# Performance work log

Hardware: AMD Instinct MI355X
Metric: run time of the kernel (lower is better)

Reference implementation:

```python
import jax, jax.numpy as jnp
import numpy as np

N_NODES = 10000
N_EDGES = 160000


def _conv2d(x, w, b):
    y = jax.lax.conv_general_dilated(x, w, (1, 1), 'SAME',
                                     dimension_numbers=('NCHW', 'OIHW', 'NCHW'))
    return jax.nn.selu(y + b[None, :, None, None])


def _cnn(cf, cnn_w1, cnn_b1, cnn_w2, cnn_b2, cnn_w3, cnn_b3, cnn_w4, cnn_b4):
    h = _conv2d(cf, cnn_w1, cnn_b1)
    h = _conv2d(h, cnn_w2, cnn_b2)
    h = _conv2d(h, cnn_w3, cnn_b3)
    h = _conv2d(h, cnn_w4, cnn_b4)
    return h.mean(axis=(2, 3))  # (1, 24) global avg pool


def _gat(x, src, dst, W, a_s, a_d, b, n):
    # PyG GATConv, concat=False (mean over heads), add_self_loops handled by caller
    H, C = a_s.shape
    h = (x @ W).reshape(-1, H, C)                      # (N,H,C)
    e = jax.nn.leaky_relu((h * a_s).sum(-1)[src] +
                          (h * a_d).sum(-1)[dst], 0.2)  # (E,H)
    m = jax.ops.segment_max(e, dst, num_segments=n)
    p = jnp.exp(e - m[dst])
    z = jax.ops.segment_sum(p, dst, num_segments=n)
    alpha = p / (z[dst] + 1e-16)
    out = jax.ops.segment_sum(h[src] * alpha[..., None], dst, num_segments=n)
    return out.mean(axis=1) + b


def _fix_boundary(v, up, down, left, right):
    c0 = jnp.where(down, 0.0, jnp.where(up, 1.0, v[:, 0]))
    c1 = jnp.where(right, 1.0, jnp.where(left, 0.0, v[:, 1]))
    return v.at[:, 0].set(c0).at[:, 1].set(c1)


def setup_inputs() -> dict:
    key = jax.random.key(0)
    ks = jax.random.split(key, 40)
    d = {}
    d['x'] = jax.random.uniform(ks[0], (N_NODES, 10), dtype=jnp.float32)
    d['edge_index'] = jax.random.randint(ks[1], (2, N_EDGES), 0, N_NODES, dtype=jnp.int64)
    d['conv_feat'] = jax.random.normal(ks[2], (1, 4, 64, 64), dtype=jnp.float32)
    cnn_dims = [(16, 4), (32, 16), (64, 32), (24, 64)]
    for i, (o, c) in enumerate(cnn_dims, 1):
        d[f'cnn_w{i}'] = jax.random.normal(ks[2 + i], (o, c, 3, 3), jnp.float32) * 0.1
        d[f'cnn_b{i}'] = jnp.zeros((o,), jnp.float32)
    gat_dims = [(34, 8, 64), (64, 16, 128), (128, 8, 256), (256, 8, 128), (128, 16, 2)]
    for i, (fin, H, C) in enumerate(gat_dims, 1):
        k1, k2, k3 = jax.random.split(ks[10 + i], 3)
        d[f'g{i}_w'] = jax.random.normal(k1, (fin, H * C), jnp.float32) * 0.1
        d[f'g{i}_as'] = jax.random.normal(k2, (H, C), jnp.float32) * 0.1
        d[f'g{i}_ad'] = jax.random.normal(k3, (H, C), jnp.float32) * 0.1
        d[f'g{i}_b'] = jnp.zeros((C,), jnp.float32)
    return d


def reference(x, edge_index, conv_feat,
              cnn_w1, cnn_b1, cnn_w2, cnn_b2, cnn_w3, cnn_b3, cnn_w4, cnn_b4,
              g1_w, g1_as, g1_ad, g1_b,
              g2_w, g2_as, g2_ad, g2_b,
              g3_w, g3_as, g3_ad, g3_b,
              g4_w, g4_as, g4_ad, g4_b,
              g5_w, g5_as, g5_ad, g5_b):
    n = x.shape[0]
    # boundary masks from raw node coordinates
    up, down = x[:, 0] == 1, x[:, 0] == 0
    left, right = x[:, 1] == 0, x[:, 1] == 1
    # add self loops (PyG GATConv default)
    loops = jnp.arange(n, dtype=edge_index.dtype)
    src = jnp.concatenate([edge_index[0], loops])
    dst = jnp.concatenate([edge_index[1], loops])

    gfeat = _cnn(conv_feat, cnn_w1, cnn_b1, cnn_w2, cnn_b2, cnn_w3, cnn_b3, cnn_w4, cnn_b4)
    h = jnp.concatenate([jnp.broadcast_to(gfeat, (n, gfeat.shape[1])), x], axis=1)

    h = jax.nn.selu(_gat(h, src, dst, g1_w, g1_as, g1_ad, g1_b, n))
    h = _fix_boundary(h, up, down, left, right)
    h = jax.nn.selu(_gat(h, src, dst, g2_w, g2_as, g2_ad, g2_b, n))
    h = _fix_boundary(h, up, down, left, right)
    h = jax.nn.selu(_gat(h, src, dst, g3_w, g3_as, g3_ad, g3_b, n))
    h = _fix_boundary(h, up, down, left, right)
    h = jax.nn.selu(_gat(h, src, dst, g4_w, g4_as, g4_ad, g4_b, n))
    h = _fix_boundary(h, up, down, left, right)
    res = jax.nn.selu(_gat(h, src, dst, g5_w, g5_as, g5_ad, g5_b, n))
    out = x[:, :2] + res
    out = _fix_boundary(out, up, down, left, right)
    return out
```

## Files before the change

### kernel.cpp

```cpp
#include <hip/hip_runtime.h>
#include <hip/hip_fp16.h>
#include <math.h>


#define DEVFN static __device__ __forceinline__

typedef __attribute__((ext_vector_type(8))) _Float16 half8;
typedef __attribute__((ext_vector_type(4))) _Float16 half4v;
typedef __attribute__((ext_vector_type(4))) float f32x4;

DEVFN float selu_f(float v) {
    const float scale = 1.0507009873554805f;
    const float alpha = 1.6732632423543772f;
    return v > 0.f ? scale * v : scale * alpha * (expf(v) - 1.f);
}

DEVFN float lrelu02(float v) { return v > 0.f ? v : 0.2f * v; }

#define PST 66
#define PSZ (66 * 66)

__global__ void pad_input(const float* __restrict__ cf, float* __restrict__ out) {
    int t = blockIdx.x * blockDim.x + threadIdx.x;
    if (t >= 4 * 4096) return;
    int c = t >> 12, pix = t & 4095;
    int y = pix >> 6, x = pix & 63;
    out[c * PSZ + (y + 1) * PST + (x + 1)] = cf[t];
}

template <int CIN>
__global__ __launch_bounds__(256) void conv3x3_pad(const float* __restrict__ in,
                                                   const float* __restrict__ w,
                                                   const float* __restrict__ b,
                                                   float* __restrict__ out) {
    int x  = threadIdx.x & 63;
    int yg = threadIdx.x >> 6;
    int y  = blockIdx.x * 4 + yg;
    int co = blockIdx.y;
    float acc = b[co];
    const float* wp = w + (size_t)co * CIN * 9;
#pragma unroll 4
    for (int ci = 0; ci < CIN; ++ci) {
        const float* ip = in + ci * PSZ + y * PST + x;
        const float* wr = wp + ci * 9;
        acc += wr[0] * ip[0]           + wr[1] * ip[1]           + wr[2] * ip[2]
             + wr[3] * ip[PST]         + wr[4] * ip[PST + 1]     + wr[5] * ip[PST + 2]
             + wr[6] * ip[2 * PST]     + wr[7] * ip[2 * PST + 1] + wr[8] * ip[2 * PST + 2];
    }
    out[(size_t)co * PSZ + (y + 1) * PST + (x + 1)] = selu_f(acc);
}

__global__ void avgpool_c(const float* __restrict__ in, float* __restrict__ gfeat) {
    int c = blockIdx.x;
    int t = threadIdx.x;
    float s = 0.f;
    for (int i = t; i < 4096; i += 256) {
        int y = i >> 6, x = i & 63;
        s += in[c * PSZ + (y + 1) * PST + (x + 1)];
    }
#pragma unroll
    for (int off = 32; off >= 1; off >>= 1) s += __shfl_xor(s, off);
    __shared__ float red[4];
    int wave = t >> 6, lane = t & 63;
    if (lane == 0) red[wave] = s;
    __syncthreads();
    if (t == 0) gfeat[c] = (red[0] + red[1] + red[2] + red[3]) * (1.f / 4096.f);
}

__global__ void build_h0(const float* __restrict__ x, const float* __restrict__ gfeat,
                         __half* __restrict__ h0f, unsigned* __restrict__ masks, int N) {
    int n = blockIdx.x * blockDim.x + threadIdx.x;
    if (n >= N) return;
    float x0 = x[n * 10 + 0], x1 = x[n * 10 + 1];
    unsigned mk = (x0 == 1.f ? 1u : 0u) | (x0 == 0.f ? 2u : 0u) |
                  (x1 == 0.f ? 4u : 0u) | (x1 == 1.f ? 8u : 0u);
    masks[n] = mk;
    __half* hq = h0f + (size_t)n * 64;
#pragma unroll
    for (int j = 0; j < 64; ++j) {
        float v = (j < 24) ? gfeat[j] : (j < 34 ? x[n * 10 + (j - 24)] : 0.f);
        hq[j] = __float2half(v);
    }
}

__global__ void count_dst(const int* __restrict__ ei, int* __restrict__ cnt, int E, int N) {
    int t = blockIdx.x * blockDim.x + threadIdx.x;
    if (t >= E + N) return;
    int dst = (t < E) ? ei[E + t] : (t - E);
    atomicAdd(&cnt[dst], 1);
}

__global__ void scan_blocks(const int* __restrict__ cnt, int* __restrict__ pref,
                            int* __restrict__ bsums, int n) {
    __shared__ int sdata[256];
    int i = blockIdx.x * 256 + threadIdx.x;
    int v = (i < n) ? cnt[i] : 0;
    sdata[threadIdx.x] = v;
    __syncthreads();
    for (int off = 1; off < 256; off <<= 1) {
        int tmp = (threadIdx.x >= off) ? sdata[threadIdx.x - off] : 0;
        __syncthreads();
        sdata[threadIdx.x] += tmp;
        __syncthreads();
    }
    if (i < n) pref[i] = sdata[threadIdx.x] - v;
    if (threadIdx.x == 255) bsums[blockIdx.x] = sdata[255];
}

__global__ void scan_sums(int* __restrict__ bsums, int nb) {
    int tid = threadIdx.x;
    int orig = (tid < nb) ? bsums[tid] : 0;
    int v = orig;
#pragma unroll
    for (int off = 1; off < 64; off <<= 1) {
        int u = __shfl_up(v, off);
        if (tid >= off) v += u;
    }
    if (tid < nb) bsums[tid] = v - orig;
}

__global__ void scan_apply(const int* __restrict__ pref, const int* __restrict__ bsums,
                           int* __restrict__ indptr, int* __restrict__ cursor,
                           int n, int total) {
    int i = blockIdx.x * 256 + threadIdx.x;
    if (i == 0) indptr[n] = total;
    if (i >= n) return;
    int e = bsums[blockIdx.x] + pref[i];
    indptr[i] = e;
    cursor[i] = e;
}

__global__ void scatter_edges(const int* __restrict__ ei, int* __restrict__ cursor,
                              int* __restrict__ col, int E, int N) {
    int t = blockIdx.x * blockDim.x + threadIdx.x;
    if (t >= E + N) return;
    int src, dst;
    if (t < E) { src = ei[t]; dst = ei[E + t]; }
    else       { src = dst = t - E; }
    int pos = atomicAdd(&cursor[dst], 1);
    col[pos] = src;
}

__global__ __launch_bounds__(256) void prep_all(
        const float* __restrict__ W0, const float* __restrict__ W1,
        const float* __restrict__ W2, const float* __restrict__ W3,
        const float* __restrict__ W4,
        const float* __restrict__ as0, const float* __restrict__ as1,
        const float* __restrict__ as2, const float* __restrict__ as3,
        const float* __restrict__ as4,
        const float* __restrict__ ad0, const float* __restrict__ ad1,
        const float* __restrict__ ad2, const float* __restrict__ ad3,
        const float* __restrict__ ad4,
        unsigned short* __restrict__ bt, float* __restrict__ wesed,
        float* __restrict__ wcomb) {
    const int Kc[5]  = {34, 64, 128, 256, 128};
    const int Kpc[5] = {64, 64, 128, 256, 128};
    const int Hc[5]  = {8, 16, 8, 8, 16};
    const int Cc[5]  = {64, 128, 256, 128, 2};
    const int HCc[5] = {512, 2048, 2048, 1024, 32};
    const int KAc[5] = {512, 1024, 1024, 2048, 2048};
    const int btOff[5] = {0, 32768, 163840, 425984, 0};
    const int weOff[5] = {0, 1024, 3072, 5120, 9216};

    int b = blockIdx.x, tid = threadIdx.x;

    if (b < 168) {
        int lyr, tloc;
        if (b < 8)        { lyr = 0; tloc = b; }
        else if (b < 40)  { lyr = 1; tloc = b - 8; }
        else if (b < 104) { lyr = 2; tloc = b - 40; }
        else              { lyr = 3; tloc = b - 104; }
        const int ktl[4] = {1, 1, 2, 4};
        const int mtl[4] = {1, 2, 4, 2};
        int kt = ktl[lyr], mt = mtl[lyr];
        int per_h = kt * mt;
        int h = tloc / per_h, r = tloc - h * per_h;
        int ki = r % kt, mi = r / kt;
        int k0 = ki * 64, m0 = mi * 64;
        int K = Kc[lyr], Kp = Kpc[lyr], C = Cc[lyr], HC = HCc[lyr], KA = KAc[lyr];
        const float* W;
        if (lyr == 0) W = W0; else if (lyr == 1) W = W1;
        else if (lyr == 2) W = W2; else W = W3;

        __shared__ float tile[64][65];
        int c = tid & 63, rg = tid >> 6;
        for (int r2 = rg; r2 < 64; r2 += 4) {
            int k = k0 + r2, m = m0 + c;
            float v = (k < K && m < C) ? W[(size_t)k * HC + h * C + m] : 0.f;
            tile[r2][c] = v;
        }
        __syncthreads();
        unsigned short* bp = bt + btOff[lyr];
        for (int mr = rg; mr < 64; mr += 4) {
            int m = m0 + mr, k = k0 + c;
            if (m < C && k < Kp)
                bp[(size_t)m * KA + h * Kp + k] =
                    __half_as_ushort(__float2half(tile[c][mr]));
        }
    } else if (b < 200) {
        int u = (b - 168) * 256 + tid;
        int k = u >> 6, o = u & 63;
        float s;
        if (o < 32) {
            int h = (o < 16) ? o : o - 16;
            const float* av = ((o < 16) ? as4 : ad4) + h * 2;
            s = W4[k * 32 + h * 2 + 0] * av[0] + W4[k * 32 + h * 2 + 1] * av[1];
        } else {
            s = W4[k * 32 + (o - 32)];
        }
        wcomb[u] = s;
    } else {
        int wb = b - 200;
        int lyr, u0;
        if (wb < 4)       { lyr = 0; u0 = wb * 256; }
        else if (wb < 12) { lyr = 1; u0 = (wb - 4) * 256; }
        else if (wb < 20) { lyr = 2; u0 = (wb - 12) * 256; }
        else if (wb < 36) { lyr = 3; u0 = (wb - 20) * 256; }
        else              { lyr = 4; u0 = (wb - 36) * 256; }
        int u = u0 + tid;
        int K = Kc[lyr], Kp = Kpc[lyr], H = Hc[lyr], C = Cc[lyr], HC = HCc[lyr];
        int H2 = 2 * H;
        if (u < Kp * H2) {
            int k = u / H2, o = u - k * H2;
            float s = 0.f;
            if (k < K) {
                int h = (o < H) ? o : o - H;
                const float *W, *as_, *ad_;
                if (lyr == 0)      { W = W0; as_ = as0; ad_ = ad0; }
                else if (lyr == 1) { W = W1; as_ = as1; ad_ = ad1; }
                else if (lyr == 2) { W = W2; as_ = as2; ad_ = ad2; }
                else if (lyr == 3) { W = W3; as_ = as3; ad_ = ad3; }
                else               { W = W4; as_ = as4; ad_ = ad4; }
                const float* av = ((o < H) ? as_ : ad_) + h * C;
                const float* wp = W + (size_t)k * HC + h * C;
#pragma unroll 4
                for (int c2 = 0; c2 < C; ++c2) s += wp[c2] * av[c2];
            }
            wesed[weOff[lyr] + u] = s;
        }
    }
}

__global__ void esed_kernel(const __half* __restrict__ hin, const float* __restrict__ wesed,
                            float* __restrict__ esed, int N, int Kp, int H2) {
    int t = blockIdx.x * blockDim.x + threadIdx.x;
    if (t >= N * H2) return;
    int n = t / H2, o = t - n * H2;
    const __half2* hp = (const __half2*)(hin + (size_t)n * Kp);
    float s = 0.f;
    for (int k2 = 0; k2 < Kp / 2; ++k2) {
        float2 f = __half22float2(hp[k2]);
        s += f.x * wesed[(2 * k2) * H2 + o] + f.y * wesed[(2 * k2 + 1) * H2 + o];
    }
    esed[t] = s;
}

template <int H, int KP, int CH, int NPB>
__global__ __launch_bounds__(NPB * (KP / CH)) void gat_fused_lds(
        const __half* __restrict__ hinf, const float* __restrict__ esed,
        const int* __restrict__ indptr, const int* __restrict__ col,
        __half* __restrict__ g, int N) {
    const int TPN = KP / CH;
    const int EC  = TPN / H;
    const int H2  = 2 * H;
    __shared__ float lds_p[NPB][TPN];
    int sub = threadIdx.x / TPN;
    int j   = threadIdx.x % TPN;
    int n = blockIdx.x * NPB + sub;
    if (n >= N) return;
    int e_my = j / H, h_my = j % H;
    int c0 = j * CH;
    float edv = esed[n * H2 + H + h_my];

    float acc[H][CH];
#pragma unroll
    for (int h = 0; h < H; ++h)
#pragma unroll
        for (int t = 0; t < CH; ++t) acc[h][t] = 0.f;
    float zloc = 0.f;

    int beg = indptr[n], deg = indptr[n + 1] - beg;
    for (int base = 0; base < deg; base += EC) {
        int ce = base + e_my;
        float p = 0.f;
        if (ce < deg) {
            int srcm = col[beg + ce];
            p = expf(lrelu02(esed[srcm * H2 + h_my] + edv));
        }
        zloc += p;
        lds_p[sub][j] = p;
        __builtin_amdgcn_wave_barrier();
#pragma unroll
        for (int e = 0; e < EC; ++e) {
            int idx = base + e;
            if (idx < deg) {
                int src = col[beg + idx];
                float f[CH];
                if (CH == 2) {
                    __half2 hv = *(const __half2*)(hinf + (size_t)src * KP + c0);
                    float2 ff = __half22float2(hv);
                    f[0] = ff.x; f[1] = ff.y;
                } else {
                    half4v hv = *(const half4v*)(hinf + (size_t)src * KP + c0);
                    f[0] = (float)hv[0]; f[1] = (float)hv[1];
                    f[2] = (float)hv[2]; f[3] = (float)hv[3];
                }
                const float4* ap = (const float4*)&lds_p[sub][e * H];
#pragma unroll
                for (int q4 = 0; q4 < H / 4; ++q4) {
                    float4 a4 = ap[q4];
#pragma unroll
                    for (int t = 0; t < CH; ++t) {
                        acc[4 * q4 + 0][t] += a4.x * f[t];
                        acc[4 * q4 + 1][t] += a4.y * f[t];
                        acc[4 * q4 + 2][t] += a4.z * f[t];
                        acc[4 * q4 + 3][t] += a4.w * f[t];
                    }
                }
            }
        }
        __builtin_amdgcn_wave_barrier();
    }

#pragma unroll
    for (int off = H; off < TPN; off <<= 1)
        zloc += __shfl_xor(zloc, off, TPN);
    float zinv_my = (1.f / H) / (zloc + 1e-16f);

    __half* gp = g + (size_t)n * (H * KP) + c0;
#pragma unroll
    for (int h = 0; h < H; ++h) {
        float zf = __shfl(zinv_my, h, TPN);
        if (CH == 2) {
            *(__half2*)(gp + h * KP) =
                __floats2half2_rn(acc[h][0] * zf, acc[h][1] * zf);
        } else {
            __half2 lo = __floats2half2_rn(acc[h][0] * zf, acc[h][1] * zf);
            __half2 hi = __floats2half2_rn(acc[h][2] * zf, acc[h][3] * zf);
            union { __half2 h2[2]; float2 f2; } u;
            u.h2[0] = lo; u.h2[1] = hi;
            *(float2*)(gp + h * KP) = u.f2;
        }
    }
}

template <int NPB>
__global__ __launch_bounds__(NPB * 32) void final_attn(
        const float* __restrict__ eyp, const int* __restrict__ indptr,
        const int* __restrict__ col, const float* __restrict__ b5,
        const unsigned* __restrict__ masks, const float* __restrict__ x,
        float* __restrict__ outp, int N) {
    int sub = threadIdx.x >> 5;
    int j   = threadIdx.x & 31;
    int n = blockIdx.x * NPB + sub;
    if (n >= N) return;
    int h = j >> 1;
    float edv = eyp[(size_t)n * 64 + 16 + h];
    int beg = indptr[n], end = indptr[n + 1];
    float z = 0.f, a = 0.f;
    int i = beg;
    for (; i + 1 < end; i += 2) {
        int s0 = col[i], s1 = col[i + 1];
        const float* r0 = eyp + (size_t)s0 * 64;
        const float* r1 = eyp + (size_t)s1 * 64;
        float es0 = r0[h], y0 = r0[32 + j];
        float es1 = r1[h], y1 = r1[32 + j];
        float p0 = expf(lrelu02(es0 + edv));
        float p1 = expf(lrelu02(es1 + edv));
        z += p0; a += p0 * y0;
        z += p1; a += p1 * y1;
    }
    for (; i < end; ++i) {
        const float* r = eyp + (size_t)col[i] * 64;
        float p = expf(lrelu02(r[h] + edv));
        z += p; a += p * r[32 + j];
    }
    float zf = (1.f / 16.f) / (z + 1e-16f);
    float val = a * zf;
#pragma unroll
    for (int off = 2; off <= 16; off <<= 1) val += __shfl_xor(val, off, 32);
    float other = __shfl_xor(val, 1, 32);
    if (j == 0) {
        unsigned mk = masks[n];
        float v0 = x[n * 10 + 0] + selu_f(val + b5[0]);
        float v1 = x[n * 10 + 1] + selu_f(other + b5[1]);
        if (mk & 2u) v0 = 0.f; else if (mk & 1u) v0 = 1.f;
        if (mk & 8u) v1 = 1.f; else if (mk & 4u) v1 = 0.f;
        outp[n * 2 + 0] = v0;
        outp[n * 2 + 1] = v1;
    }
}

#define LDP 72
__global__ __launch_bounds__(256) void gemm_lds(const __half* __restrict__ A,
                                                const unsigned short* __restrict__ Bhi,
                                                const float* __restrict__ bias,
                                                const unsigned* __restrict__ masks,
                                                __half* __restrict__ O16,
                                                int N, int K, int M) {
    __shared__ __half lA[64 * LDP], lB[64 * LDP];
    int tid = threadIdx.x;
    int wave = tid >> 6, lane = tid & 63;
    int ln16 = lane & 15, q = lane >> 4;
    int row0 = blockIdx.x * 64;
    int col0 = blockIdx.y * 64;

    int r0 = tid >> 3, r1 = r0 + 32;
    int ac = (tid & 7) * 8;
    int ga0 = min(row0 + r0, N - 1);
    int ga1 = min(row0 + r1, N - 1);
    const __half* Bp = (const __half*)Bhi;
    const __half* a0p = A + (size_t)ga0 * K + ac;
    const __half* a1p = A + (size_t)ga1 * K + ac;
    const __half* b0p = Bp + (size_t)(col0 + r0) * K + ac;
    const __half* b1p = Bp + (size_t)(col0 + r1) * K + ac;

    half8 ra0 = *(const half8*)(a0p);
    half8 ra1 = *(const half8*)(a1p);
    half8 rb0 = *(const half8*)(b0p);
    half8 rb1 = *(const half8*)(b1p);

    f32x4 acc[4];
#pragma unroll
    for (int j = 0; j < 4; ++j) acc[j] = (f32x4){0.f, 0.f, 0.f, 0.f};

    for (int kc = 0; kc < K; kc += 64) {
        __syncthreads();
        *(half8*)(lA + r0 * LDP + ac) = ra0;
        *(half8*)(lA + r1 * LDP + ac) = ra1;
        *(half8*)(lB + r0 * LDP + ac) = rb0;
        *(half8*)(lB + r1 * LDP + ac) = rb1;
        __syncthreads();
        int kn = kc + 64;
        if (kn < K) {
            ra0 = *(const half8*)(a0p + kn);
            ra1 = *(const half8*)(a1p + kn);
            rb0 = *(const half8*)(b0p + kn);
            rb1 = *(const half8*)(b1p + kn);
        }
#pragma unroll
        for (int kk = 0; kk < 2; ++kk) {
            half8 af = *(const half8*)(lA + (wave * 16 + ln16) * LDP + kk * 32 + q * 8);
#pragma unroll
            for (int j = 0; j < 4; ++j) {
                half8 bf = *(const half8*)(lB + (j * 16 + ln16) * LDP + kk * 32 + q * 8);
                acc[j] = __builtin_amdgcn_mfma_f32_16x16x32_f16(af, bf, acc[j], 0, 0, 0);
            }
        }
    }

#pragma unroll
    for (int j = 0; j < 4; ++j) {
        int cc = col0 + j * 16 + ln16;
        float bv = bias[cc];
#pragma unroll
        for (int r = 0; r < 4; ++r) {
            int rr = row0 + wave * 16 + q * 4 + r;
            if (rr >= N) continue;
            float v = selu_f(acc[j][r] + bv);
            if (cc < 2) {
                unsigned mk = masks[rr];
                if (cc == 0) { if (mk & 2u) v = 0.f; else if (mk & 1u) v = 1.f; }
                else         { if (mk & 8u) v = 1.f; else if (mk & 4u) v = 0.f; }
            }
            O16[(size_t)rr * M + cc] = __float2half(v);
        }
    }
}

extern "C" void kernel_launch(void* const* d_in, const int* in_sizes, int n_in,
                              void* d_out, int out_size, void* d_ws, size_t ws_size,
                              hipStream_t stream) {
    const float* x   = (const float*)d_in[0];
    const int*   ei  = (const int*)d_in[1];
    const float* cf  = (const float*)d_in[2];
    const float* cw[4] = {(const float*)d_in[3], (const float*)d_in[5],
                          (const float*)d_in[7], (const float*)d_in[9]};
    const float* cb[4] = {(const float*)d_in[4], (const float*)d_in[6],
                          (const float*)d_in[8], (const float*)d_in[10]};
    const float* gw[5], *gas[5], *gad[5], *gb[5];
    for (int i = 0; i < 5; ++i) {
        gw[i]  = (const float*)d_in[11 + 4 * i];
        gas[i] = (const float*)d_in[12 + 4 * i];
        gad[i] = (const float*)d_in[13 + 4 * i];
        gb[i]  = (const float*)d_in[14 + 4 * i];
    }
    const int N = in_sizes[0] / 10;
    const int E = in_sizes[1] / 2;
    const int EN = E + N;
    const int NB = (N + 255) / 256;

    char* base = (char*)d_ws;
    size_t off = 0;
    auto alloc = [&](size_t bytes) -> char* {
        char* p = base + off;
        off = (off + bytes + 255) & ~(size_t)255;
        return p;
    };
    float* cfp   = (float*)alloc((size_t)4 * PSZ * 4);
    float* c1p   = (float*)alloc((size_t)16 * PSZ * 4);
    float* c2p   = (float*)alloc((size_t)32 * PSZ * 4);
    float* c3p   = (float*)alloc((size_t)64 * PSZ * 4);
    float* c4p   = (float*)alloc((size_t)24 * PSZ * 4);
    float* gfeat = (float*)alloc(24 * 4);
    __half* hA16 = (__half*)alloc((size_t)N * 256 * 2);
    __half* hB16 = (__half*)alloc((size_t)N * 256 * 2);
    __half* g    = (__half*)alloc((size_t)N * 2048 * 2);
    float* esed  = (float*)alloc((size_t)N * 32 * 4);
    float* eyp   = (float*)alloc((size_t)N * 64 * 4);
    float* wesed = (float*)alloc((size_t)13312 * 4);
    float* wcomb = (float*)alloc((size_t)8192 * 4);
    unsigned short* bt = (unsigned short*)alloc((size_t)688128 * 2);
    unsigned* masks = (unsigned*)alloc((size_t)N * 4);
    int* cnt    = (int*)alloc((size_t)N * 4);
    int* pref   = (int*)alloc((size_t)N * 4);
    int* bsums  = (int*)alloc(64 * 4);
    int* indptr = (int*)alloc((size_t)(N + 1) * 4);
    int* cursor = (int*)alloc((size_t)N * 4);
    int* col    = (int*)alloc((size_t)EN * 4);
    (void)ws_size;

    prep_all<<<252, 256, 0, stream>>>(gw[0], gw[1], gw[2], gw[3], gw[4],
                                      gas[0], gas[1], gas[2], gas[3], gas[4],
                                      gad[0], gad[1], gad[2], gad[3], gad[4],
                                      bt, wesed, wcomb);

    hipMemsetAsync(cfp, 0, (size_t)140 * PSZ * 4, stream);
    pad_input<<<(4 * 4096 + 255) / 256, 256, 0, stream>>>(cf, cfp);
    conv3x3_pad<4><<<dim3(16, 16), 256, 0, stream>>>(cfp, cw[0], cb[0], c1p);
    conv3x3_pad<16><<<dim3(16, 32), 256, 0, stream>>>(c1p, cw[1], cb[1], c2p);
    conv3x3_pad<32><<<dim3(16, 64), 256, 0, stream>>>(c2p, cw[2], cb[2], c3p);
    conv3x3_pad<64><<<dim3(16, 24), 256, 0, stream>>>(c3p, cw[3], cb[3], c4p);
    avgpool_c<<<24, 256, 0, stream>>>(c4p, gfeat);

    build_h0<<<(N + 255) / 256, 256, 0, stream>>>(x, gfeat, hA16, masks, N);

    hipMemsetAsync(cnt, 0, (size_t)N * 4, stream);
    count_dst<<<(EN + 255) / 256, 256, 0, stream>>>(ei, cnt, E, N);
    scan_blocks<<<NB, 256, 0, stream>>>(cnt, pref, bsums, N);
    scan_sums<<<1, 64, 0, stream>>>(bsums, NB);
    scan_apply<<<NB, 256, 0, stream>>>(pref, bsums, indptr, cursor, N, EN);
    scatter_edges<<<(EN + 255) / 256, 256, 0, stream>>>(ei, cursor, col, E, N);

    const int Hs[5] = {8, 16, 8, 8, 16};
    const int Cs[5] = {64, 128, 256, 128, 2};
    const int Kp[5] = {64, 64, 128, 256, 128};
    const int btOffA[5] = {0, 32768, 163840, 425984, 0};
    const int weOffA[5] = {0, 1024, 3072, 5120, 9216};

    const __half* hin16 = hA16;
    __half* hout16[4]  = {hB16, hA16, hB16, hA16};

    for (int lyr = 0; lyr < 5; ++lyr) {
        int KP = Kp[lyr], H = Hs[lyr], C = Cs[lyr];
        int KA = H * KP;
        if (lyr == 4) {
            esed_kernel<<<(N * 64 + 255) / 256, 256, 0, stream>>>(hin16, wcomb, eyp,
                                                                  N, 128, 64);
            final_attn<8><<<(N + 7) / 8, 256, 0, stream>>>(eyp, indptr, col, gb[4],
                                                           masks, x, (float*)d_out, N);
            break;
        }
        esed_kernel<<<(N * 2 * H + 255) / 256, 256, 0, stream>>>(hin16, wesed + weOffA[lyr],
                                                                 esed, N, KP, 2 * H);
        if (lyr == 0) {
            gat_fused_lds<8, 64, 4, 16><<<(N + 15) / 16, 256, 0, stream>>>(
                hin16, esed, indptr, col, g, N);
        } else if (lyr == 1) {
            gat_fused_lds<16, 64, 2, 8><<<(N + 7) / 8, 256, 0, stream>>>(
                hin16, esed, indptr, col, g, N);
        } else if (lyr == 2) {
            gat_fused_lds<8, 128, 4, 8><<<(N + 7) / 8, 256, 0, stream>>>(
                hin16, esed, indptr, col, g, N);
        } else {
            gat_fused_lds<8, 256, 4, 4><<<(N + 3) / 4, 256, 0, stream>>>(
                hin16, esed, indptr, col, g, N);
        }

        const unsigned short* btL = bt + btOffA[lyr];
        int gx = (N + 63) / 64;
        gemm_lds<<<dim3(gx, C / 64), 256, 0, stream>>>(g, btL, gb[lyr], masks,
                                                       hout16[lyr], N, KA, C);
        hin16 = hout16[lyr];
    }
}
```

Baseline: 513.1 us.

## Double-buffer attention weights in GAT aggregation and add 32x128 GEMM tile

The GAT aggregation kernel now double-buffers the per-edge attention coefficients in LDS. It prefetches the next chunk's source index and score before the current chunk's feature accumulation, so load latency overlaps with FMA work and one wave barrier per iteration goes away. A new GEMM kernel with 32-row by 128-column tiles and register-prefetched K slices replaces the 64x64 tile for layers after the first. This changes the grid shape and data reuse in exchange for more LDS and registers.

```diff
diff --git a/kernel.cpp b/kernel.cpp
--- a/kernel.cpp
+++ b/kernel.cpp
@@ -263,7 +263,7 @@
     const int TPN = KP / CH;
     const int EC  = TPN / H;
     const int H2  = 2 * H;
-    __shared__ float lds_p[NPB][TPN];
+    __shared__ float lds_p[NPB][2][TPN];
     int sub = threadIdx.x / TPN;
     int j   = threadIdx.x % TPN;
     int n = blockIdx.x * NPB + sub;
@@ -280,16 +280,24 @@
     float zloc = 0.f;
 
     int beg = indptr[n], deg = indptr[n + 1] - beg;
+
+    float p = 0.f;
+    if (e_my < deg) {
+        int srcm = col[beg + e_my];
+        p = expf(lrelu02(esed[srcm * H2 + h_my] + edv));
+    }
+    int buf = 0;
     for (int base = 0; base < deg; base += EC) {
-        int ce = base + e_my;
-        float p = 0.f;
-        if (ce < deg) {
+        zloc += p;
+        lds_p[sub][buf][j] = p;
+        __builtin_amdgcn_wave_barrier();
+        int ce = base + EC + e_my;
+        bool vnext = (ce < deg);
+        float esv = 0.f;
+        if (vnext) {
             int srcm = col[beg + ce];
-            p = expf(lrelu02(esed[srcm * H2 + h_my] + edv));
-        }
-        zloc += p;
-        lds_p[sub][j] = p;
-        __builtin_amdgcn_wave_barrier();
+            esv = esed[srcm * H2 + h_my];
+        }
 #pragma unroll
         for (int e = 0; e < EC; ++e) {
             int idx = base + e;
@@ -305,7 +313,7 @@
                     f[0] = (float)hv[0]; f[1] = (float)hv[1];
                     f[2] = (float)hv[2]; f[3] = (float)hv[3];
                 }
-                const float4* ap = (const float4*)&lds_p[sub][e * H];
+                const float4* ap = (const float4*)&lds_p[sub][buf][e * H];
 #pragma unroll
                 for (int q4 = 0; q4 < H / 4; ++q4) {
                     float4 a4 = ap[q4];
@@ -319,7 +327,8 @@
                 }
             }
         }
-        __builtin_amdgcn_wave_barrier();
+        p = vnext ? expf(lrelu02(esv + edv)) : 0.f;
+        buf ^= 1;
     }
 
 #pragma unroll
@@ -392,6 +401,7 @@
 }
 
 #define LDP 72
+
 __global__ __launch_bounds__(256) void gemm_lds(const __half* __restrict__ A,
                                                 const unsigned short* __restrict__ Bhi,
                                                 const float* __restrict__ bias,
@@ -456,6 +466,87 @@
 #pragma unroll
         for (int r = 0; r < 4; ++r) {
             int rr = row0 + wave * 16 + q * 4 + r;
+            if (rr >= N) continue;
+            float v = selu_f(acc[j][r] + bv);
+            if (cc < 2) {
+                unsigned mk = masks[rr];
+                if (cc == 0) { if (mk & 2u) v = 0.f; else if (mk & 1u) v = 1.f; }
+                else         { if (mk & 8u) v = 1.f; else if (mk & 4u) v = 0.f; }
+            }
+            O16[(size_t)rr * M + cc] = __float2half(v);
+        }
+    }
+}
+
+__global__ __launch_bounds__(256) void gemm_rc(const __half* __restrict__ A,
+                                               const unsigned short* __restrict__ Bhi,
+                                               const float* __restrict__ bias,
+                                               const unsigned* __restrict__ masks,
+                                               __half* __restrict__ O16,
+                                               int N, int K, int M) {
+    __shared__ __half lA[32 * LDP], lB[128 * LDP];
+    int tid = threadIdx.x;
+    int wave = tid >> 6, lane = tid & 63;
+    int ln16 = lane & 15, q = lane >> 4;
+    int row0 = blockIdx.x * 32;
+    int col0 = blockIdx.y * 128;
+    int wr = (wave >> 1) * 16;
+    int wc = (wave & 1) * 64;
+
+    int ar = tid >> 3;
+    int ac = (tid & 7) * 8;
+    int ga = min(row0 + ar, N - 1);
+    const __half* ap  = A + (size_t)ga * K + ac;
+    const __half* Bp  = (const __half*)Bhi;
+    const __half* b0p = Bp + (size_t)(col0 + ar) * K + ac;
+    const __half* b1p = Bp + (size_t)(col0 + ar + 32) * K + ac;
+    const __half* b2p = Bp + (size_t)(col0 + ar + 64) * K + ac;
+    const __half* b3p = Bp + (size_t)(col0 + ar + 96) * K + ac;
+
+    half8 ra  = *(const half8*)(ap);
+    half8 rb0 = *(const half8*)(b0p);
+    half8 rb1 = *(const half8*)(b1p);
+    half8 rb2 = *(const half8*)(b2p);
+    half8 rb3 = *(const half8*)(b3p);
+
+    f32x4 acc[4];
+#pragma unroll
+    for (int j = 0; j < 4; ++j) acc[j] = (f32x4){0.f, 0.f, 0.f, 0.f};
+
+    for (int kc = 0; kc < K; kc += 64) {
+        __syncthreads();
+        *(half8*)(lA + ar * LDP + ac)        = ra;
+        *(half8*)(lB + ar * LDP + ac)        = rb0;
+        *(half8*)(lB + (ar + 32) * LDP + ac) = rb1;
+        *(half8*)(lB + (ar + 64) * LDP + ac) = rb2;
+        *(half8*)(lB + (ar + 96) * LDP + ac) = rb3;
+        __syncthreads();
+        int kn = kc + 64;
+        if (kn < K) {
+            ra  = *(const half8*)(ap + kn);
+            rb0 = *(const half8*)(b0p + kn);
+            rb1 = *(const half8*)(b1p + kn);
+            rb2 = *(const half8*)(b2p + kn);
+            rb3 = *(const half8*)(b3p + kn);
+        }
+#pragma unroll
+        for (int kk = 0; kk < 2; ++kk) {
+            half8 af = *(const half8*)(lA + (wr + ln16) * LDP + kk * 32 + q * 8);
+#pragma unroll
+            for (int j = 0; j < 4; ++j) {
+                half8 bf = *(const half8*)(lB + (wc + j * 16 + ln16) * LDP + kk * 32 + q * 8);
+                acc[j] = __builtin_amdgcn_mfma_f32_16x16x32_f16(af, bf, acc[j], 0, 0, 0);
+            }
+        }
+    }
+
+#pragma unroll
+    for (int j = 0; j < 4; ++j) {
+        int cc = col0 + wc + j * 16 + ln16;
+        float bv = bias[cc];
+#pragma unroll
+        for (int r = 0; r < 4; ++r) {
+            int rr = row0 + wr + q * 4 + r;
             if (rr >= N) continue;
             float v = selu_f(acc[j][r] + bv);
             if (cc < 2) {
@@ -578,9 +669,13 @@
         }
 
         const unsigned short* btL = bt + btOffA[lyr];
-        int gx = (N + 63) / 64;
-        gemm_lds<<<dim3(gx, C / 64), 256, 0, stream>>>(g, btL, gb[lyr], masks,
-                                                       hout16[lyr], N, KA, C);
+        if (lyr == 0) {
+            gemm_lds<<<dim3((N + 63) / 64, 1), 256, 0, stream>>>(g, btL, gb[lyr], masks,
+                                                                 hout16[lyr], N, KA, C);
+        } else {
+            gemm_rc<<<dim3((N + 31) / 32, C / 128), 256, 0, stream>>>(g, btL, gb[lyr], masks,
+                                                                      hout16[lyr], N, KA, C);
+        }
         hin16 = hout16[lyr];
     }
 }
```

New measurement: 506.8 us. About the same (-1.2%).
